# Kernel optimization log

Measured on AMD Instinct MI355X. Metric: run time of the kernel, lower is better.

## Reference

```python
import jax, jax.numpy as jnp
import numpy as np

B = 262144
NUM_FEA = 32
EMB_DIM = 8
OUT_DIM = 16

def setup_inputs() -> dict:
    key = jax.random.key(0)
    ks = jax.random.split(key, 6)
    x = jax.random.normal(ks[0], (B, NUM_FEA), dtype=jnp.float32)
    # per-feature Dense(1 -> emb_dim): weight row + bias per feature
    emb_W = jax.random.normal(ks[1], (NUM_FEA, EMB_DIM), dtype=jnp.float32) * 0.5
    emb_b = jax.random.normal(ks[2], (NUM_FEA, EMB_DIM), dtype=jnp.float32) * 0.1
    M = jax.random.normal(ks[3], (EMB_DIM, EMB_DIM), dtype=jnp.float32) * (1.0 / np.sqrt(EMB_DIM))
    dense_W = jax.random.normal(ks[4], (NUM_FEA, OUT_DIM), dtype=jnp.float32) * (1.0 / np.sqrt(NUM_FEA))
    dense_b = jax.random.normal(ks[5], (OUT_DIM,), dtype=jnp.float32) * 0.1
    return {"x": x, "emb_W": emb_W, "emb_b": emb_b, "M": M,
            "dense_W": dense_W, "dense_b": dense_b}

def reference(x, emb_W, emb_b, M, dense_W, dense_b):
    mid = x.shape[1] // 2  # 16
    # fused batched per-feature Dense(1 -> emb_dim): [B, F, E]
    emb = x[:, :, None] * emb_W[None, :, :] + emb_b[None, :, :]
    left = emb[:, :mid, :]    # [B, mid, E]
    right = emb[:, mid:, :]   # [B, mid, E]
    # bilinear co-attention: G = tanh(left @ M @ right^T), [B, mid, mid]
    G = jnp.tanh(jnp.einsum('ble,ef,brf->blr', left, M, right))
    lr = jax.nn.softmax(G.sum(axis=1), axis=-1)  # [B, mid]
    rl = jax.nn.softmax(G.sum(axis=2), axis=-1)  # [B, mid]
    a = jnp.concatenate([lr, rl], axis=-1)       # [B, F]
    out = x * a
    # mix == 'concat': Dense(16, relu)
    return jax.nn.relu(out @ dense_W + dense_b)
```

## Files before the change

### kernel.cpp

```cpp
#include <hip/hip_runtime.h>
#include <hip/hip_bf16.h>


typedef __attribute__((ext_vector_type(2))) float v2f;

#if __has_builtin(__builtin_amdgcn_exp2f)
#define EXP2F(v) __builtin_amdgcn_exp2f(v)
#else
#define EXP2F(v) exp2f(v)
#endif

#if __has_builtin(__builtin_amdgcn_rcpf)
#define RCPF(v) __builtin_amdgcn_rcpf(v)
#else
#define RCPF(v) (1.0f / (v))
#endif

#define LOG2E 1.4426950408889634f

__device__ __forceinline__ v2f fma2(v2f a, v2f b, v2f c) {
    return __builtin_elementwise_fma(a, b, c);
}

__global__ __launch_bounds__(256) void coattn_setup(
    const float* __restrict__ emb_W,
    const float* __restrict__ emb_b,
    const float* __restrict__ M,
    float* __restrict__ C)
{
    const int t = threadIdx.x;
    const int l = t >> 4;
    const int r = t & 15;

    float MW[8], Mb[8];
    #pragma unroll
    for (int e = 0; e < 8; ++e) {
        float s1 = 0.0f, s2 = 0.0f;
        #pragma unroll
        for (int f = 0; f < 8; ++f) {
            float m = M[e * 8 + f];
            s1 = fmaf(m, emb_W[(16 + r) * 8 + f], s1);
            s2 = fmaf(m, emb_b[(16 + r) * 8 + f], s2);
        }
        MW[e] = s1; Mb[e] = s2;
    }
    float c1 = 0.0f, c2 = 0.0f, c3 = 0.0f, c4 = 0.0f;
    #pragma unroll
    for (int e = 0; e < 8; ++e) {
        float w = emb_W[l * 8 + e];
        float b = emb_b[l * 8 + e];
        c1 = fmaf(w, MW[e], c1);
        c2 = fmaf(w, Mb[e], c2);
        c3 = fmaf(b, MW[e], c3);
        c4 = fmaf(b, Mb[e], c4);
    }
    const float s = 2.0f * LOG2E;
    C[0 * 256 + l * 16 + r] = c1 * s;
    C[1 * 256 + l * 16 + r] = c2 * s;
    C[2 * 256 + l * 16 + r] = c3 * s;
    C[3 * 256 + l * 16 + r] = c4 * s;
}

__global__ __launch_bounds__(256) void coattn_kernel(
    const float* __restrict__ x,
    const float* __restrict__ C,
    const float* __restrict__ dW,
    const float* __restrict__ db,
    float* __restrict__ out)
{
    #pragma clang fp contract(off)

    const int i = blockIdx.x * blockDim.x + threadIdx.x;

    v2f xv2[16];
    const float4* xp = reinterpret_cast<const float4*>(x + (size_t)i * 32);
    #pragma unroll
    for (int k = 0; k < 8; ++k) {
        float4 v = xp[k];
        xv2[2*k+0] = (v2f){v.x, v.y};
        xv2[2*k+1] = (v2f){v.z, v.w};
    }

    const v2f* C1 = reinterpret_cast<const v2f*>(C);
    const v2f* C2 = C1 + 128;
    const v2f* C3 = C2 + 128;
    const v2f* C4 = C3 + 128;

    v2f Scol[8];
    #pragma unroll
    for (int k = 0; k < 8; ++k) Scol[k] = (v2f){0.0f, 0.0f};
    float Srow[16];

    #pragma unroll
    for (int l = 0; l < 16; ++l) {
        const float xl = xv2[l >> 1][l & 1];
        const v2f xl2 = (v2f){xl, xl};
        v2f rs = (v2f){0.0f, 0.0f};
        #pragma unroll
        for (int k = 0; k < 8; ++k) {
            const v2f xr2 = xv2[8 + k];
            v2f u = xl2 * C1[l * 8 + k];
            u = u + C3[l * 8 + k];
            v2f w = xl2 * C2[l * 8 + k];
            w = w + C4[l * 8 + k];
            v2f g = fma2(xr2, u, w);
            v2f E;
            E.x = EXP2F(g.x);
            E.y = EXP2F(g.y);
            v2f D = E + 1.0f;
            v2f rc;
            rc.x = RCPF(D.x);
            rc.y = RCPF(D.y);
            Scol[k] = Scol[k] + rc;
            rs = rs + rc;
        }
        Srow[l] = rs.x + rs.y;
    }

    const float NSCL = -2.0f * LOG2E;
    v2f av[16];
    {
        float s = 0.0f;
        #pragma unroll
        for (int k = 0; k < 8; ++k) {
            v2f arg = Scol[k] * NSCL;
            v2f e;
            e.x = EXP2F(arg.x);
            e.y = EXP2F(arg.y);
            av[k] = e;
            s += e.x + e.y;
        }
        float inv = RCPF(s);
        #pragma unroll
        for (int k = 0; k < 8; ++k) av[k] = av[k] * inv;
    }
    {
        float s = 0.0f;
        #pragma unroll
        for (int m = 0; m < 8; ++m) {
            v2f sr = (v2f){Srow[2*m], Srow[2*m+1]};
            v2f arg = sr * NSCL;
            v2f e;
            e.x = EXP2F(arg.x);
            e.y = EXP2F(arg.y);
            av[8 + m] = e;
            s += e.x + e.y;
        }
        float inv = RCPF(s);
        #pragma unroll
        for (int m = 0; m < 8; ++m) av[8 + m] = av[8 + m] * inv;
    }

    v2f xa[16];
    #pragma unroll
    for (int m = 0; m < 16; ++m) xa[m] = xv2[m] * av[m];

    const v2f* dW2 = reinterpret_cast<const v2f*>(dW);
    const v2f* db2 = reinterpret_cast<const v2f*>(db);
    v2f o2[8];
    #pragma unroll
    for (int m = 0; m < 8; ++m) o2[m] = db2[m];
    #pragma unroll
    for (int j = 0; j < 32; ++j) {
        const float xj = xa[j >> 1][j & 1];
        const v2f xj2 = (v2f){xj, xj};
        #pragma unroll
        for (int m = 0; m < 8; ++m)
            o2[m] = fma2(xj2, dW2[j * 8 + m], o2[m]);
    }

    float4* op = reinterpret_cast<float4*>(out + (size_t)i * 16);
    #pragma unroll
    for (int t = 0; t < 4; ++t) {
        v2f a0 = __builtin_elementwise_max(o2[2*t+0], (v2f){0.0f, 0.0f});
        v2f a1 = __builtin_elementwise_max(o2[2*t+1], (v2f){0.0f, 0.0f});
        float4 v;
        v.x = a0.x; v.y = a0.y; v.z = a1.x; v.w = a1.y;
        op[t] = v;
    }
}

extern "C" void kernel_launch(void* const* d_in, const int* in_sizes, int n_in,
                              void* d_out, int out_size, void* d_ws, size_t ws_size,
                              hipStream_t stream) {
    const float* x     = (const float*)d_in[0];
    const float* emb_W = (const float*)d_in[1];
    const float* emb_b = (const float*)d_in[2];
    const float* M     = (const float*)d_in[3];
    const float* dW    = (const float*)d_in[4];
    const float* db    = (const float*)d_in[5];
    float* out = (float*)d_out;
    float* C   = (float*)d_ws;

    hipLaunchKernelGGL(coattn_setup, dim3(1), dim3(256), 0, stream,
                       emb_W, emb_b, M, C);

    const int B = in_sizes[0] / 32;
    dim3 block(256);
    dim3 grid((B + 255) / 256);
    hipLaunchKernelGGL(coattn_kernel, grid, block, 0, stream,
                       x, C, dW, db, out);
}
```

Before: 104.7 us.

## Split each sample across two wavefronts and combine partial sums via LDS

```diff
diff --git a/kernel.cpp b/kernel.cpp
--- a/kernel.cpp
+++ b/kernel.cpp
@@ -61,7 +61,54 @@
     C[3 * 256 + l * 16 + r] = c4 * s;
 }
 
-__global__ __launch_bounds__(256) void coattn_kernel(
+template<int P>
+__device__ __forceinline__ void dense_tail(
+    const v2f (&xl2)[4], const v2f (&xr2)[8], const v2f (&elr)[8],
+    float invlr, float invrl, const float (&er)[8],
+    const v2f* __restrict__ dW2, const v2f* __restrict__ db2v,
+    v2f* __restrict__ slot,
+    v2f& r0, v2f& r1, v2f& r2, v2f& r3)
+{
+    v2f xa[8];
+    #pragma unroll
+    for (int i = 0; i < 4; ++i)
+        xa[i] = xl2[i] * (elr[4 * P + i] * invlr);
+    #pragma unroll
+    for (int i = 0; i < 4; ++i) {
+        v2f a; a.x = er[2 * i] * invrl; a.y = er[2 * i + 1] * invrl;
+        xa[4 + i] = xr2[4 * P + i] * a;
+    }
+
+    v2f o2[8];
+    #pragma unroll
+    for (int m = 0; m < 8; ++m) o2[m] = (v2f){0.0f, 0.0f};
+    #pragma unroll
+    for (int m = 0; m < 4; ++m) o2[4 * P + m] = db2v[4 * P + m];
+
+    #pragma unroll
+    for (int i2 = 0; i2 < 8; ++i2) {
+        const float xj = xa[i2 >> 1][i2 & 1];
+        const v2f xj2 = (v2f){xj, xj};
+        const v2f* row = dW2 + (8 * P + i2) * 8;
+        #pragma unroll
+        for (int m = 0; m < 8; ++m) o2[m] = fma2(xj2, row[m], o2[m]);
+    }
+    #pragma unroll
+    for (int i2 = 0; i2 < 8; ++i2) {
+        const float xj = xa[4 + (i2 >> 1)][i2 & 1];
+        const v2f xj2 = (v2f){xj, xj};
+        const v2f* row = dW2 + (16 + 8 * P + i2) * 8;
+        #pragma unroll
+        for (int m = 0; m < 8; ++m) o2[m] = fma2(xj2, row[m], o2[m]);
+    }
+
+    #pragma unroll
+    for (int m = 0; m < 4; ++m) slot[m] = o2[4 * (1 - P) + m];
+    r0 = o2[4 * P + 0]; r1 = o2[4 * P + 1];
+    r2 = o2[4 * P + 2]; r3 = o2[4 * P + 3];
+}
+
+__global__ __launch_bounds__(128, 8) void coattn_kernel(
     const float* __restrict__ x,
     const float* __restrict__ C,
     const float* __restrict__ dW,
@@ -70,47 +117,50 @@
 {
     #pragma clang fp contract(off)
 
-    const int i = blockIdx.x * blockDim.x + threadIdx.x;
-
-    v2f xv2[16];
-    const float4* xp = reinterpret_cast<const float4*>(x + (size_t)i * 32);
-    #pragma unroll
-    for (int k = 0; k < 8; ++k) {
-        float4 v = xp[k];
-        xv2[2*k+0] = (v2f){v.x, v.y};
-        xv2[2*k+1] = (v2f){v.z, v.w};
-    }
-
-    const v2f* C1 = reinterpret_cast<const v2f*>(C);
-    const v2f* C2 = C1 + 128;
-    const v2f* C3 = C2 + 128;
-    const v2f* C4 = C3 + 128;
+    __shared__ float ldsS[128 * 16];
+    __shared__ float ldsP[128];
+
+    const int tid  = threadIdx.x;
+    const int lane = tid & 63;
+    const int p    = __builtin_amdgcn_readfirstlane(tid >> 6);
+    const long e   = (long)blockIdx.x * 64 + lane;
+
+    v2f xl2[4], xr2[8];
+    {
+        const float4* xp = reinterpret_cast<const float4*>(x + e * 32);
+        float4 a0 = xp[2 * p], a1 = xp[2 * p + 1];
+        xl2[0] = (v2f){a0.x, a0.y}; xl2[1] = (v2f){a0.z, a0.w};
+        xl2[2] = (v2f){a1.x, a1.y}; xl2[3] = (v2f){a1.z, a1.w};
+        #pragma unroll
+        for (int k = 0; k < 4; ++k) {
+            float4 v = xp[4 + k];
+            xr2[2*k] = (v2f){v.x, v.y}; xr2[2*k+1] = (v2f){v.z, v.w};
+        }
+    }
+
+    const v2f* C1 = reinterpret_cast<const v2f*>(C) + p * 64;
+    const v2f* C2 = reinterpret_cast<const v2f*>(C) + 128 + p * 64;
+    const v2f* C3 = reinterpret_cast<const v2f*>(C) + 256 + p * 64;
+    const v2f* C4 = reinterpret_cast<const v2f*>(C) + 384 + p * 64;
 
     v2f Scol[8];
     #pragma unroll
     for (int k = 0; k < 8; ++k) Scol[k] = (v2f){0.0f, 0.0f};
-    float Srow[16];
-
-    #pragma unroll
-    for (int l = 0; l < 16; ++l) {
-        const float xl = xv2[l >> 1][l & 1];
-        const v2f xl2 = (v2f){xl, xl};
+    float Srow[8];
+
+    #pragma unroll
+    for (int l = 0; l < 8; ++l) {
+        const float xl_ = xl2[l >> 1][l & 1];
+        const v2f xlv = (v2f){xl_, xl_};
         v2f rs = (v2f){0.0f, 0.0f};
         #pragma unroll
         for (int k = 0; k < 8; ++k) {
-            const v2f xr2 = xv2[8 + k];
-            v2f u = xl2 * C1[l * 8 + k];
-            u = u + C3[l * 8 + k];
-            v2f w = xl2 * C2[l * 8 + k];
-            w = w + C4[l * 8 + k];
-            v2f g = fma2(xr2, u, w);
-            v2f E;
-            E.x = EXP2F(g.x);
-            E.y = EXP2F(g.y);
+            v2f u = xlv * C1[l * 8 + k]; u = u + C3[l * 8 + k];
+            v2f w = xlv * C2[l * 8 + k]; w = w + C4[l * 8 + k];
+            v2f g = fma2(xr2[k], u, w);
+            v2f E; E.x = EXP2F(g.x); E.y = EXP2F(g.y);
             v2f D = E + 1.0f;
-            v2f rc;
-            rc.x = RCPF(D.x);
-            rc.y = RCPF(D.y);
+            v2f rc; rc.x = RCPF(D.x); rc.y = RCPF(D.y);
             Scol[k] = Scol[k] + rc;
             rs = rs + rc;
         }
@@ -118,65 +168,63 @@
     }
 
     const float NSCL = -2.0f * LOG2E;
-    v2f av[16];
-    {
-        float s = 0.0f;
-        #pragma unroll
-        for (int k = 0; k < 8; ++k) {
-            v2f arg = Scol[k] * NSCL;
-            v2f e;
-            e.x = EXP2F(arg.x);
-            e.y = EXP2F(arg.y);
-            av[k] = e;
-            s += e.x + e.y;
-        }
-        float inv = RCPF(s);
-        #pragma unroll
-        for (int k = 0; k < 8; ++k) av[k] = av[k] * inv;
-    }
-    {
-        float s = 0.0f;
-        #pragma unroll
-        for (int m = 0; m < 8; ++m) {
-            v2f sr = (v2f){Srow[2*m], Srow[2*m+1]};
-            v2f arg = sr * NSCL;
-            v2f e;
-            e.x = EXP2F(arg.x);
-            e.y = EXP2F(arg.y);
-            av[8 + m] = e;
-            s += e.x + e.y;
-        }
-        float inv = RCPF(s);
-        #pragma unroll
-        for (int m = 0; m < 8; ++m) av[8 + m] = av[8 + m] * inv;
-    }
-
-    v2f xa[16];
-    #pragma unroll
-    for (int m = 0; m < 16; ++m) xa[m] = xv2[m] * av[m];
-
-    const v2f* dW2 = reinterpret_cast<const v2f*>(dW);
-    const v2f* db2 = reinterpret_cast<const v2f*>(db);
-    v2f o2[8];
-    #pragma unroll
-    for (int m = 0; m < 8; ++m) o2[m] = db2[m];
-    #pragma unroll
-    for (int j = 0; j < 32; ++j) {
-        const float xj = xa[j >> 1][j & 1];
-        const v2f xj2 = (v2f){xj, xj};
-        #pragma unroll
-        for (int m = 0; m < 8; ++m)
-            o2[m] = fma2(xj2, dW2[j * 8 + m], o2[m]);
-    }
-
-    float4* op = reinterpret_cast<float4*>(out + (size_t)i * 16);
-    #pragma unroll
-    for (int t = 0; t < 4; ++t) {
-        v2f a0 = __builtin_elementwise_max(o2[2*t+0], (v2f){0.0f, 0.0f});
-        v2f a1 = __builtin_elementwise_max(o2[2*t+1], (v2f){0.0f, 0.0f});
-        float4 v;
-        v.x = a0.x; v.y = a0.y; v.z = a1.x; v.w = a1.y;
-        op[t] = v;
+    float er[8], pd = 0.0f;
+    #pragma unroll
+    for (int l = 0; l < 8; ++l) { er[l] = EXP2F(Srow[l] * NSCL); pd += er[l]; }
+
+    {
+        v2f* myS = reinterpret_cast<v2f*>(ldsS + tid * 16);
+        #pragma unroll
+        for (int k = 0; k < 8; ++k) myS[k] = Scol[k];
+        ldsP[tid] = pd;
+    }
+    __syncthreads();
+    float denr;
+    {
+        const int q = tid ^ 64;
+        const v2f* pS = reinterpret_cast<const v2f*>(ldsS + q * 16);
+        #pragma unroll
+        for (int k = 0; k < 8; ++k) Scol[k] = Scol[k] + pS[k];
+        denr = pd + ldsP[q];
+    }
+
+    v2f elr[8];
+    float s = 0.0f;
+    #pragma unroll
+    for (int k = 0; k < 8; ++k) {
+        v2f arg = Scol[k] * NSCL;
+        v2f ee; ee.x = EXP2F(arg.x); ee.y = EXP2F(arg.y);
+        elr[k] = ee;
+        s += ee.x + ee.y;
+    }
+    const float invlr = RCPF(s);
+    const float invrl = RCPF(denr);
+
+    __syncthreads();
+
+    const v2f* dW2  = reinterpret_cast<const v2f*>(dW);
+    const v2f* db2v = reinterpret_cast<const v2f*>(db);
+    v2f* slot = reinterpret_cast<v2f*>(ldsS + tid * 16);
+    v2f r0, r1, r2, r3;
+    if (p == 0)
+        dense_tail<0>(xl2, xr2, elr, invlr, invrl, er, dW2, db2v, slot, r0, r1, r2, r3);
+    else
+        dense_tail<1>(xl2, xr2, elr, invlr, invrl, er, dW2, db2v, slot, r0, r1, r2, r3);
+
+    __syncthreads();
+
+    {
+        const v2f* ps = reinterpret_cast<const v2f*>(ldsS + (tid ^ 64) * 16);
+        v2f z = (v2f){0.0f, 0.0f};
+        v2f f0 = __builtin_elementwise_max(r0 + ps[0], z);
+        v2f f1 = __builtin_elementwise_max(r1 + ps[1], z);
+        v2f f2 = __builtin_elementwise_max(r2 + ps[2], z);
+        v2f f3 = __builtin_elementwise_max(r3 + ps[3], z);
+        float4* op = reinterpret_cast<float4*>(out + e * 16 + p * 8);
+        float4 v0; v0.x = f0.x; v0.y = f0.y; v0.z = f1.x; v0.w = f1.y;
+        float4 v1; v1.x = f2.x; v1.y = f2.y; v1.z = f3.x; v1.w = f3.y;
+        op[0] = v0;
+        op[1] = v1;
     }
 }
 
@@ -196,8 +244,8 @@
                        emb_W, emb_b, M, C);
 
     const int B = in_sizes[0] / 32;
-    dim3 block(256);
-    dim3 grid((B + 255) / 256);
+    dim3 block(128);
+    dim3 grid(B / 64);
     hipLaunchKernelGGL(coattn_kernel, grid, block, 0, stream,
                        x, C, dW, db, out);
 }
```

New measurement: 106.8 us. 1.02x slower.

## Pair reciprocals in sigmoid loop and force packed-FP32 ops with SGPR constants

Applied to the files above, without the earlier changes.

```diff
diff --git a/kernel.cpp b/kernel.cpp
--- a/kernel.cpp
+++ b/kernel.cpp
@@ -18,8 +18,23 @@
 
 #define LOG2E 1.4426950408889634f
 
-__device__ __forceinline__ v2f fma2(v2f a, v2f b, v2f c) {
-    return __builtin_elementwise_fma(a, b, c);
+__device__ __forceinline__ v2f pk_mul_vs(v2f a, v2f s) {
+    v2f d; asm("v_pk_mul_f32 %0, %1, %2" : "=v"(d) : "v"(a), "s"(s)); return d;
+}
+__device__ __forceinline__ v2f pk_add_vs(v2f a, v2f s) {
+    v2f d; asm("v_pk_add_f32 %0, %1, %2" : "=v"(d) : "v"(a), "s"(s)); return d;
+}
+__device__ __forceinline__ v2f pk_fma_vvv(v2f a, v2f b, v2f c) {
+    v2f d; asm("v_pk_fma_f32 %0, %1, %2, %3" : "=v"(d) : "v"(a), "v"(b), "v"(c)); return d;
+}
+__device__ __forceinline__ v2f pk_fma_vsv(v2f a, v2f s, v2f c) {
+    v2f d; asm("v_pk_fma_f32 %0, %1, %2, %3" : "=v"(d) : "v"(a), "s"(s), "v"(c)); return d;
+}
+__device__ __forceinline__ v2f pk_add_vv(v2f a, v2f b) {
+    v2f d; asm("v_pk_add_f32 %0, %1, %2" : "=v"(d) : "v"(a), "v"(b)); return d;
+}
+__device__ __forceinline__ v2f pk_mul_vv(v2f a, v2f b) {
+    v2f d; asm("v_pk_mul_f32 %0, %1, %2" : "=v"(d) : "v"(a), "v"(b)); return d;
 }
 
 __global__ __launch_bounds__(256) void coattn_setup(
@@ -81,38 +96,38 @@
         xv2[2*k+1] = (v2f){v.z, v.w};
     }
 
-    const v2f* C1 = reinterpret_cast<const v2f*>(C);
-    const v2f* C2 = C1 + 128;
-    const v2f* C3 = C2 + 128;
-    const v2f* C4 = C3 + 128;
+    const v2f* Cv = reinterpret_cast<const v2f*>(C);
 
     v2f Scol[8];
     #pragma unroll
     for (int k = 0; k < 8; ++k) Scol[k] = (v2f){0.0f, 0.0f};
     float Srow[16];
+    const v2f CLAMP = (v2f){88.0f, 88.0f};
 
     #pragma unroll
     for (int l = 0; l < 16; ++l) {
-        const float xl = xv2[l >> 1][l & 1];
-        const v2f xl2 = (v2f){xl, xl};
+        const float xls = xv2[l >> 1][l & 1];
+        const v2f xlv = (v2f){xls, xls};
         v2f rs = (v2f){0.0f, 0.0f};
+        const v2f* C1p = Cv + 0 * 128 + l * 8;
+        const v2f* C2p = Cv + 1 * 128 + l * 8;
+        const v2f* C3p = Cv + 2 * 128 + l * 8;
+        const v2f* C4p = Cv + 3 * 128 + l * 8;
         #pragma unroll
         for (int k = 0; k < 8; ++k) {
-            const v2f xr2 = xv2[8 + k];
-            v2f u = xl2 * C1[l * 8 + k];
-            u = u + C3[l * 8 + k];
-            v2f w = xl2 * C2[l * 8 + k];
-            w = w + C4[l * 8 + k];
-            v2f g = fma2(xr2, u, w);
-            v2f E;
-            E.x = EXP2F(g.x);
-            E.y = EXP2F(g.y);
-            v2f D = E + 1.0f;
-            v2f rc;
-            rc.x = RCPF(D.x);
-            rc.y = RCPF(D.y);
-            Scol[k] = Scol[k] + rc;
-            rs = rs + rc;
+            v2f u = pk_mul_vs(xlv, C1p[k]);
+            u = pk_add_vs(u, C3p[k]);
+            v2f q = pk_mul_vs(xlv, C2p[k]);
+            q = pk_add_vs(q, C4p[k]);
+            v2f g = pk_fma_vvv(xv2[8 + k], u, q);
+            g = __builtin_elementwise_min(g, CLAMP);
+            v2f D;
+            D.x = EXP2F(g.x) + 1.0f;
+            D.y = EXP2F(g.y) + 1.0f;
+            float t = RCPF(D.x * D.y);
+            v2f rc; rc.x = D.y * t; rc.y = D.x * t;
+            Scol[k] = pk_add_vv(Scol[k], rc);
+            rs = pk_add_vv(rs, rc);
         }
         Srow[l] = rs.x + rs.y;
     }
@@ -123,59 +138,58 @@
         float s = 0.0f;
         #pragma unroll
         for (int k = 0; k < 8; ++k) {
-            v2f arg = Scol[k] * NSCL;
-            v2f e;
-            e.x = EXP2F(arg.x);
-            e.y = EXP2F(arg.y);
-            av[k] = e;
-            s += e.x + e.y;
+            float e0 = EXP2F(Scol[k].x * NSCL);
+            float e1 = EXP2F(Scol[k].y * NSCL);
+            av[k] = (v2f){e0, e1};
+            s += e0 + e1;
         }
         float inv = RCPF(s);
         #pragma unroll
-        for (int k = 0; k < 8; ++k) av[k] = av[k] * inv;
+        for (int k = 0; k < 8; ++k) { av[k].x *= inv; av[k].y *= inv; }
     }
     {
         float s = 0.0f;
+        float er[16];
+        #pragma unroll
+        for (int l = 0; l < 16; ++l) { er[l] = EXP2F(Srow[l] * NSCL); s += er[l]; }
+        float inv = RCPF(s);
+        #pragma unroll
+        for (int m = 0; m < 8; ++m)
+            av[8 + m] = (v2f){er[2*m] * inv, er[2*m+1] * inv};
+    }
+
+    v2f xa2[16];
+    #pragma unroll
+    for (int m = 0; m < 16; ++m) xa2[m] = pk_mul_vv(xv2[m], av[m]);
+
+    const v2f* dW2  = reinterpret_cast<const v2f*>(dW);
+    const v2f* db2v = reinterpret_cast<const v2f*>(db);
+    v2f o2[8];
+    #pragma unroll
+    for (int m = 0; m < 8; ++m) o2[m] = db2v[m];
+
+    #pragma unroll
+    for (int jp = 0; jp < 16; ++jp) {
+        const v2f xa = xa2[jp];
+        const v2f lo = (v2f){xa.x, xa.x};
+        const v2f hi = (v2f){xa.y, xa.y};
+        const v2f* w0 = dW2 + (2 * jp + 0) * 8;
+        const v2f* w1 = dW2 + (2 * jp + 1) * 8;
         #pragma unroll
         for (int m = 0; m < 8; ++m) {
-            v2f sr = (v2f){Srow[2*m], Srow[2*m+1]};
-            v2f arg = sr * NSCL;
-            v2f e;
-            e.x = EXP2F(arg.x);
-            e.y = EXP2F(arg.y);
-            av[8 + m] = e;
-            s += e.x + e.y;
-        }
-        float inv = RCPF(s);
-        #pragma unroll
-        for (int m = 0; m < 8; ++m) av[8 + m] = av[8 + m] * inv;
-    }
-
-    v2f xa[16];
-    #pragma unroll
-    for (int m = 0; m < 16; ++m) xa[m] = xv2[m] * av[m];
-
-    const v2f* dW2 = reinterpret_cast<const v2f*>(dW);
-    const v2f* db2 = reinterpret_cast<const v2f*>(db);
-    v2f o2[8];
-    #pragma unroll
-    for (int m = 0; m < 8; ++m) o2[m] = db2[m];
-    #pragma unroll
-    for (int j = 0; j < 32; ++j) {
-        const float xj = xa[j >> 1][j & 1];
-        const v2f xj2 = (v2f){xj, xj};
-        #pragma unroll
-        for (int m = 0; m < 8; ++m)
-            o2[m] = fma2(xj2, dW2[j * 8 + m], o2[m]);
+            o2[m] = pk_fma_vsv(lo, w0[m], o2[m]);
+            o2[m] = pk_fma_vsv(hi, w1[m], o2[m]);
+        }
     }
 
     float4* op = reinterpret_cast<float4*>(out + (size_t)i * 16);
     #pragma unroll
     for (int t = 0; t < 4; ++t) {
-        v2f a0 = __builtin_elementwise_max(o2[2*t+0], (v2f){0.0f, 0.0f});
-        v2f a1 = __builtin_elementwise_max(o2[2*t+1], (v2f){0.0f, 0.0f});
         float4 v;
-        v.x = a0.x; v.y = a0.y; v.z = a1.x; v.w = a1.y;
+        v.x = fmaxf(o2[2*t+0].x, 0.0f);
+        v.y = fmaxf(o2[2*t+0].y, 0.0f);
+        v.z = fmaxf(o2[2*t+1].x, 0.0f);
+        v.w = fmaxf(o2[2*t+1].y, 0.0f);
         op[t] = v;
     }
 }
```

New measurement: 109.6 us. 4.7% more time.
